# Optimization experiments

Hardware: AMD Instinct MI355X
Metric: run time of the kernel (lower is better)

## Reference

```python
import jax, jax.numpy as jnp
import numpy as np

EPS = 1e-5
OUTPUT_BINS = 1000


def _act_quant(x):
    # per-token absmax int8 quantization (BitNet b1.58)
    scale = 127.0 / jnp.clip(jnp.max(jnp.abs(x), axis=-1, keepdims=True), EPS, None)
    return jnp.clip(jnp.round(x * scale), -128.0, 127.0) / scale


def _weight_quant(w):
    # ternary absmean quantization
    scale = 1.0 / jnp.clip(jnp.mean(jnp.abs(w)), EPS, None)
    return jnp.clip(jnp.round(w * scale), -1.0, 1.0) / scale


def _ste(x, q):
    return x + jax.lax.stop_gradient(q - x)


def bitlinear(x, w):
    xq = _ste(x, _act_quant(x))
    wq = _ste(w, _weight_quant(w))
    return jnp.einsum('bi,oi->bo', xq, wq)


def layernorm(x, g, b):
    mu = jnp.mean(x, axis=-1, keepdims=True)
    var = jnp.mean(jnp.square(x - mu), axis=-1, keepdims=True)
    return (x - mu) * jax.lax.rsqrt(var + EPS) * g + b


def setup_inputs() -> dict:
    key = jax.random.key(0)
    ks = jax.random.split(key, 5)
    B, D_IN, H = 4096, 1024, 4096
    return {
        'x': jax.random.normal(ks[0], (B, D_IN), dtype=jnp.float32),
        'W0': jax.random.normal(ks[1], (H, D_IN), dtype=jnp.float32) * 0.02,
        'W1': jax.random.normal(ks[2], (H, H), dtype=jnp.float32) * 0.02,
        'W2': jax.random.normal(ks[3], (H, H), dtype=jnp.float32) * 0.02,
        'W3': jax.random.normal(ks[4], (2 * OUTPUT_BINS, H), dtype=jnp.float32) * 0.02,
        'g0': jnp.ones((H,), jnp.float32), 'b0': jnp.zeros((H,), jnp.float32),
        'g1': jnp.ones((H,), jnp.float32), 'b1': jnp.zeros((H,), jnp.float32),
        'g2': jnp.ones((H,), jnp.float32), 'b2': jnp.zeros((H,), jnp.float32),
    }


def reference(x, W0, W1, W2, W3, g0, b0, g1, b1, g2, b2):
    h = jax.nn.silu(layernorm(bitlinear(x, W0), g0, b0))
    h = jax.nn.silu(layernorm(bitlinear(h, W1), g1, b1))
    h = jax.nn.silu(layernorm(bitlinear(h, W2), g2, b2))
    out = bitlinear(h, W3)                      # [B, 2*output_bins]
    mz_logits, int_logits = jnp.split(out, 2, axis=-1)
    mz_values = jax.nn.sigmoid(mz_logits) * (OUTPUT_BINS - 1) + 1.0
    intensities = jax.nn.sigmoid(int_logits) * 100.0
    return (mz_values, intensities)
```

## Files before the change

### kernel.cpp

```cpp
#include <hip/hip_runtime.h>
#include <hip/hip_bf16.h>
#include <cstdint>
#include <cstddef>

#define EPS 1e-5f

typedef __attribute__((ext_vector_type(4))) int int32x4;

__device__ __forceinline__ float blk_sum(float v, float* s4) {
    #pragma unroll
    for (int o = 32; o; o >>= 1) v += __shfl_down(v, o, 64);
    if ((threadIdx.x & 63) == 0) s4[threadIdx.x >> 6] = v;
    __syncthreads();
    v = s4[0] + s4[1] + s4[2] + s4[3];
    __syncthreads();
    return v;
}

__device__ __forceinline__ void blk_sum2(float& a, float& b, float* s8) {
    #pragma unroll
    for (int o = 32; o; o >>= 1) {
        a += __shfl_down(a, o, 64);
        b += __shfl_down(b, o, 64);
    }
    if ((threadIdx.x & 63) == 0) {
        s8[threadIdx.x >> 6] = a;
        s8[4 + (threadIdx.x >> 6)] = b;
    }
    __syncthreads();
    a = s8[0] + s8[1] + s8[2] + s8[3];
    b = s8[4] + s8[5] + s8[6] + s8[7];
    __syncthreads();
}

__device__ __forceinline__ float blk_max(float v, float* s4) {
    #pragma unroll
    for (int o = 32; o; o >>= 1) v = fmaxf(v, __shfl_down(v, o, 64));
    if ((threadIdx.x & 63) == 0) s4[threadIdx.x >> 6] = v;
    __syncthreads();
    v = fmaxf(fmaxf(s4[0], s4[1]), fmaxf(s4[2], s4[3]));
    __syncthreads();
    return v;
}

__device__ __forceinline__ int pack4(float a, float b, float c, float d, float lo, float hi) {
    int x0 = (int)fminf(fmaxf(a, lo), hi);
    int x1 = (int)fminf(fmaxf(b, lo), hi);
    int x2 = (int)fminf(fmaxf(c, lo), hi);
    int x3 = (int)fminf(fmaxf(d, lo), hi);
    return (x0 & 255) | ((x1 & 255) << 8) | ((x2 & 255) << 16) | ((x3 & 255) << 24);
}

__device__ __forceinline__ float bflo(unsigned u) { return __uint_as_float(u << 16); }
__device__ __forceinline__ float bfhi(unsigned u) { return __uint_as_float(u & 0xffff0000u); }

__global__ __launch_bounds__(256) void absmean_all_kernel(
    const float* __restrict__ W0, const float* __restrict__ W1,
    const float* __restrict__ W2, const float* __restrict__ W3,
    float* __restrict__ part) {
    __shared__ float s4[4];
    const float* w; int sidx; unsigned rel;
    unsigned bx = blockIdx.x;
    if (bx < 1024)      { w = W0; sidx = 0; rel = bx; }
    else if (bx < 5120) { w = W1; sidx = 1; rel = bx - 1024; }
    else if (bx < 9216) { w = W2; sidx = 2; rel = bx - 5120; }
    else                { w = W3; sidx = 3; rel = bx - 9216; }
    const float4* p = (const float4*)w + (size_t)rel * 1024 + threadIdx.x;
    float4 v0 = p[0], v1 = p[256], v2 = p[512], v3 = p[768];
    float s = fabsf(v0.x) + fabsf(v0.y) + fabsf(v0.z) + fabsf(v0.w)
            + fabsf(v1.x) + fabsf(v1.y) + fabsf(v1.z) + fabsf(v1.w)
            + fabsf(v2.x) + fabsf(v2.y) + fabsf(v2.z) + fabsf(v2.w)
            + fabsf(v3.x) + fabsf(v3.y) + fabsf(v3.z) + fabsf(v3.w);
    s = blk_sum(s, s4);
    if (threadIdx.x == 0) atomicAdd(&part[(sidx * 64 + (rel & 63)) * 16], s);
}

__global__ __launch_bounds__(256) void reduce_sums_kernel(const float* __restrict__ part,
                                                          float* __restrict__ sums) {
    int w = threadIdx.x >> 6, l = threadIdx.x & 63;
    float v = part[(w * 64 + l) * 16];
    #pragma unroll
    for (int o = 32; o; o >>= 1) v += __shfl_down(v, o, 64);
    if (l == 0) sums[w] = v;
}

__global__ __launch_bounds__(256) void wquant_all_kernel(
    const float* __restrict__ W0, const float* __restrict__ W1,
    const float* __restrict__ W2, const float* __restrict__ W3,
    int* __restrict__ q0, int* __restrict__ q1, int* __restrict__ q2, int* __restrict__ q3,
    const float* __restrict__ sums) {
    const float* w; int* q; int sidx; unsigned rel; float invN; bool pad = false;
    unsigned bx = blockIdx.x;
    if (bx < 1024)      { w = W0; q = q0; sidx = 0; rel = bx;        invN = 1.f / 4194304.f; }
    else if (bx < 5120) { w = W1; q = q1; sidx = 1; rel = bx - 1024; invN = 1.f / 16777216.f; }
    else if (bx < 9216) { w = W2; q = q2; sidx = 2; rel = bx - 5120; invN = 1.f / 16777216.f; }
    else                { w = W3; q = q3; sidx = 3; rel = bx - 9216; invN = 1.f / 8192000.f;
                          pad = (rel >= 2000); }
    int4 o = {0, 0, 0, 0};
    if (!pad) {
        float mean = fmaxf(sums[sidx] * invN, EPS);
        float scale = 1.f / mean;
        const float4* p = (const float4*)w + (size_t)rel * 1024 + threadIdx.x * 4;
        float4 v0 = p[0], v1 = p[1], v2 = p[2], v3 = p[3];
        o.x = pack4(rintf(v0.x * scale), rintf(v0.y * scale), rintf(v0.z * scale), rintf(v0.w * scale), -1.f, 1.f);
        o.y = pack4(rintf(v1.x * scale), rintf(v1.y * scale), rintf(v1.z * scale), rintf(v1.w * scale), -1.f, 1.f);
        o.z = pack4(rintf(v2.x * scale), rintf(v2.y * scale), rintf(v2.z * scale), rintf(v2.w * scale), -1.f, 1.f);
        o.w = pack4(rintf(v3.x * scale), rintf(v3.y * scale), rintf(v3.z * scale), rintf(v3.w * scale), -1.f, 1.f);
    }
    ((int4*)q)[(size_t)rel * 256 + threadIdx.x] = o;
}

__global__ __launch_bounds__(256) void actquant_kernel(const float* __restrict__ x,
                                                       int* __restrict__ q,
                                                       float* __restrict__ inv_s) {
    __shared__ float s4[4];
    int row = blockIdx.x;
    const float4* xr = (const float4*)(x + (size_t)row * 1024);
    float4 v = xr[threadIdx.x];
    float m = fmaxf(fmaxf(fabsf(v.x), fabsf(v.y)), fmaxf(fabsf(v.z), fabsf(v.w)));
    m = blk_max(m, s4);
    m = fmaxf(m, EPS);
    float scale = 127.f / m;
    if (threadIdx.x == 0) inv_s[row] = m / 127.f;
    q[(size_t)row * 256 + threadIdx.x] =
        pack4(rintf(v.x * scale), rintf(v.y * scale),
              rintf(v.z * scale), rintf(v.w * scale), -128.f, 127.f);
}

__global__ __launch_bounds__(256) void ln_silu_quant_kernel(const ushort* __restrict__ h,
                                                            const float* __restrict__ g,
                                                            const float* __restrict__ b,
                                                            int* __restrict__ q,
                                                            float* __restrict__ inv_s) {
    __shared__ float s8[8];
    int row = blockIdx.x;
    int t = threadIdx.x;
    const uint4* hr = (const uint4*)(h + (size_t)row * 4096);
    uint4 p0 = hr[t * 2], p1 = hr[t * 2 + 1];
    float f[16];
    f[0] = bflo(p0.x); f[1] = bfhi(p0.x); f[2] = bflo(p0.y); f[3] = bfhi(p0.y);
    f[4] = bflo(p0.z); f[5] = bfhi(p0.z); f[6] = bflo(p0.w); f[7] = bfhi(p0.w);
    f[8] = bflo(p1.x); f[9] = bfhi(p1.x); f[10] = bflo(p1.y); f[11] = bfhi(p1.y);
    f[12] = bflo(p1.z); f[13] = bfhi(p1.z); f[14] = bflo(p1.w); f[15] = bfhi(p1.w);
    float sum = 0.f, sq = 0.f;
    #pragma unroll
    for (int i = 0; i < 16; i++) { sum += f[i]; sq += f[i] * f[i]; }
    blk_sum2(sum, sq, s8);
    float mu = sum * (1.f / 4096.f);
    float var = sq * (1.f / 4096.f) - mu * mu;
    float rs = rsqrtf(var + EPS);
    const float4* g4 = (const float4*)g;
    const float4* b4 = (const float4*)b;
    float amax = 0.f;
    #pragma unroll
    for (int i = 0; i < 4; i++) {
        float4 gg = g4[t * 4 + i];
        float4 bb = b4[t * 4 + i];
        float y0 = (f[i * 4 + 0] - mu) * rs * gg.x + bb.x;
        float y1 = (f[i * 4 + 1] - mu) * rs * gg.y + bb.y;
        float y2 = (f[i * 4 + 2] - mu) * rs * gg.z + bb.z;
        float y3 = (f[i * 4 + 3] - mu) * rs * gg.w + bb.w;
        f[i * 4 + 0] = y0 / (1.f + expf(-y0));
        f[i * 4 + 1] = y1 / (1.f + expf(-y1));
        f[i * 4 + 2] = y2 / (1.f + expf(-y2));
        f[i * 4 + 3] = y3 / (1.f + expf(-y3));
    }
    #pragma unroll
    for (int i = 0; i < 16; i++) amax = fmaxf(amax, fabsf(f[i]));
    amax = blk_max(amax, s8);
    amax = fmaxf(amax, EPS);
    float scale = 127.f / amax;
    if (t == 0) inv_s[row] = amax / 127.f;
    int4 o;
    o.x = pack4(rintf(f[0] * scale), rintf(f[1] * scale), rintf(f[2] * scale), rintf(f[3] * scale), -128.f, 127.f);
    o.y = pack4(rintf(f[4] * scale), rintf(f[5] * scale), rintf(f[6] * scale), rintf(f[7] * scale), -128.f, 127.f);
    o.z = pack4(rintf(f[8] * scale), rintf(f[9] * scale), rintf(f[10] * scale), rintf(f[11] * scale), -128.f, 127.f);
    o.w = pack4(rintf(f[12] * scale), rintf(f[13] * scale), rintf(f[14] * scale), rintf(f[15] * scale), -128.f, 127.f);
    ((int4*)((char*)q + (size_t)row * 4096))[t] = o;
}

__device__ __forceinline__ void load_lds16(const void* g, void* l) {
    __builtin_amdgcn_global_load_lds((__attribute__((address_space(1))) void*)(g),
                                     (__attribute__((address_space(3))) void*)(l), 16, 0, 0);
}

template <int MODE>
__global__ __launch_bounds__(256, 2) void gemm_i8_kernel(
    const char* __restrict__ A, const char* __restrict__ B,
    const float* __restrict__ inv_s, const float* __restrict__ wsum, float invWN,
    int K, void* __restrict__ outp) {
    __shared__ __align__(16) char lA[128 * 128];
    __shared__ __align__(16) char lB[128 * 128];
    const int t = threadIdx.x;
    const int lane = t & 63;
    const int wave = t >> 6;
    const int bm = blockIdx.y * 128, bn = blockIdx.x * 128;
    const int wr = (wave >> 1) * 64, wc = (wave & 1) * 64;

    int32x4 acc[4][4] = {};

    const int r0 = t >> 3;
    const int c0 = (t & 7) * 16;
    const int gcol = c0 ^ (16 * (r0 & 7));
    const char* gA = A + (size_t)(bm + r0) * K + gcol;
    const char* gB = B + (size_t)(bn + r0) * K + gcol;
    char* sA = lA + t * 16;
    char* sB = lB + t * 16;

    const int fr = lane & 15;
    const int fq = lane >> 4;
    const int swz = 16 * (fr & 7);

    for (int k0 = 0; k0 < K; k0 += 128) {
        #pragma unroll
        for (int j = 0; j < 4; j++)
            load_lds16(gA + (size_t)(j * 32) * K + k0, sA + j * 4096);
        #pragma unroll
        for (int j = 0; j < 4; j++)
            load_lds16(gB + (size_t)(j * 32) * K + k0, sB + j * 4096);
        __syncthreads();

        #pragma unroll
        for (int ks = 0; ks < 2; ks++) {
            const int col = (ks * 64 + fq * 16) ^ swz;
            int32x4 af[4], bf[4];
            #pragma unroll
            for (int mt = 0; mt < 4; mt++)
                af[mt] = *(const int32x4*)(lA + (wr + mt * 16 + fr) * 128 + col);
            #pragma unroll
            for (int nt = 0; nt < 4; nt++)
                bf[nt] = *(const int32x4*)(lB + (wc + nt * 16 + fr) * 128 + col);
            #pragma unroll
            for (int mt = 0; mt < 4; mt++) {
                #pragma unroll
                for (int nt = 0; nt < 4; nt++) {
                    acc[mt][nt] = __builtin_amdgcn_mfma_i32_16x16x64_i8(af[mt], bf[nt],
                                                                        acc[mt][nt], 0, 0, 0);
                }
            }
        }
        __syncthreads();
    }

    const float wmean = fmaxf(wsum[0] * invWN, EPS);
    #pragma unroll
    for (int mt = 0; mt < 4; mt++) {
        #pragma unroll
        for (int rg = 0; rg < 4; rg++) {
            int gr = bm + wr + mt * 16 + fq * 4 + rg;
            float rowscale = inv_s[gr] * wmean;
            #pragma unroll
            for (int nt = 0; nt < 4; nt++) {
                int gc = bn + wc + nt * 16 + fr;
                float v = (float)acc[mt][nt][rg] * rowscale;
                if (MODE == 0) {
                    ((__hip_bfloat16*)outp)[(size_t)gr * 4096 + gc] = __float2bfloat16(v);
                } else {
                    if (gc < 2000) {
                        float sg = 1.f / (1.f + expf(-v));
                        float* out = (float*)outp;
                        if (gc < 1000)
                            out[(size_t)gr * 1000 + gc] = sg * 999.f + 1.f;
                        else
                            out[(size_t)4096 * 1000 + (size_t)gr * 1000 + (gc - 1000)] =
                                sg * 100.f;
                    }
                }
            }
        }
    }
}

extern "C" void kernel_launch(void* const* d_in, const int* in_sizes, int n_in,
                              void* d_out, int out_size, void* d_ws, size_t ws_size,
                              hipStream_t stream) {
    const float* x  = (const float*)d_in[0];
    const float* W0 = (const float*)d_in[1];
    const float* W1 = (const float*)d_in[2];
    const float* W2 = (const float*)d_in[3];
    const float* W3 = (const float*)d_in[4];
    const float* g0 = (const float*)d_in[5];
    const float* b0 = (const float*)d_in[6];
    const float* g1 = (const float*)d_in[7];
    const float* b1 = (const float*)d_in[8];
    const float* g2 = (const float*)d_in[9];
    const float* b2 = (const float*)d_in[10];
    float* out = (float*)d_out;

    char* ws = (char*)d_ws;
    size_t off = 0;
    auto alloc = [&](size_t bytes) -> char* {
        char* p = ws + off;
        off = (off + bytes + 255) & ~(size_t)255;
        return p;
    };
    float* part = (float*)alloc(256 * 16 * sizeof(float));
    float* sums = (float*)alloc(4 * sizeof(float));
    float* inv0 = (float*)alloc(4096 * 4);
    float* inv1 = (float*)alloc(4096 * 4);
    float* inv2 = (float*)alloc(4096 * 4);
    float* inv3 = (float*)alloc(4096 * 4);
    char* wq0 = alloc(4096ll * 1024);
    char* wq1 = alloc(4096ll * 4096);
    char* wq2 = alloc(4096ll * 4096);
    char* wq3 = alloc(2048ll * 4096);
    char* a0  = alloc(4096ll * 1024);
    char* a1  = alloc(4096ll * 4096);
    char* a2  = alloc(4096ll * 4096);
    char* h   = alloc(4096ll * 4096 * 2);
    char* a3 = a1;

    hipMemsetAsync(part, 0, 256 * 16 * sizeof(float), stream);

    absmean_all_kernel<<<11216, 256, 0, stream>>>(W0, W1, W2, W3, part);
    reduce_sums_kernel<<<1, 256, 0, stream>>>(part, sums);
    actquant_kernel<<<4096, 256, 0, stream>>>(x, (int*)a0, inv0);
    wquant_all_kernel<<<11264, 256, 0, stream>>>(W0, W1, W2, W3, (int*)wq0, (int*)wq1,
                                                 (int*)wq2, (int*)wq3, sums);

    gemm_i8_kernel<0><<<dim3(32, 32), 256, 0, stream>>>(a0, wq0, inv0, sums + 0,
                                                        1.f / 4194304.f, 1024, h);
    ln_silu_quant_kernel<<<4096, 256, 0, stream>>>((const ushort*)h, g0, b0, (int*)a1, inv1);

    gemm_i8_kernel<0><<<dim3(32, 32), 256, 0, stream>>>(a1, wq1, inv1, sums + 1,
                                                        1.f / 16777216.f, 4096, h);
    ln_silu_quant_kernel<<<4096, 256, 0, stream>>>((const ushort*)h, g1, b1, (int*)a2, inv2);

    gemm_i8_kernel<0><<<dim3(32, 32), 256, 0, stream>>>(a2, wq2, inv2, sums + 2,
                                                        1.f / 16777216.f, 4096, h);
    ln_silu_quant_kernel<<<4096, 256, 0, stream>>>((const ushort*)h, g2, b2, (int*)a3, inv3);

    gemm_i8_kernel<1><<<dim3(16, 32), 256, 0, stream>>>(a3, wq3, inv3, sums + 3,
                                                        1.f / 8192000.f, 4096, out);
}
```

Baseline: 518.0 us.

## Add 256x256-tile 512-thread int8 MFMA GEMM with LDS double buffering for hidden layers

Adds a new int8 GEMM kernel that uses 256x256 output tiles per 8-wave workgroup, double-buffered LDS staging with direct global-to-LDS loads, XOR-swizzled LDS layout, interleaved MFMA/staging phases with s_setprio, and a workgroup index remap for L2 locality. The three 4096-wide hidden-layer GEMMs switch to it, while the final output GEMM stays on the old kernel. The aim is more operand reuse per LDS byte and better overlap of global loads with MFMA compute. The trade-offs are a grid of only 256 workgroups, which may not fill the device evenly, high register pressure from 32 accumulators per thread, and hand-written waitcnt counts that depend on how the compiler orders instructions.

```diff
diff --git a/kernel.cpp b/kernel.cpp
--- a/kernel.cpp
+++ b/kernel.cpp
@@ -271,6 +271,172 @@
     }
 }
 
+template <int MH>
+__device__ __forceinline__ void mfma_quad(int32x4 (&acc)[8][4], const int32x4 (&af)[4],
+                                          const int32x4 (&bf)[4]) {
+    #pragma unroll
+    for (int i = 0; i < 4; i++) {
+        #pragma unroll
+        for (int j = 0; j < 4; j++) {
+            acc[MH * 4 + i][j] =
+                __builtin_amdgcn_mfma_i32_16x16x64_i8(af[i], bf[j], acc[MH * 4 + i][j], 0, 0, 0);
+        }
+    }
+}
+
+__global__ __launch_bounds__(512, 2) void gemm_i8_big(
+    const char* __restrict__ A, const char* __restrict__ B,
+    const float* __restrict__ inv_s, const float* __restrict__ wsum, float invWN,
+    int K, __hip_bfloat16* __restrict__ outp) {
+    __shared__ __align__(16) char lA[2][2][256][64];
+    __shared__ __align__(16) char lB[2][2][256][64];
+    const int t = threadIdx.x;
+    const int lane = t & 63;
+    const int wave = t >> 6;
+
+    const int nwg = gridDim.x * gridDim.y;
+    const int wg0 = blockIdx.y * gridDim.x + blockIdx.x;
+    const int q8 = nwg >> 3;
+    const int wg = (wg0 & 7) * q8 + (wg0 >> 3);
+    const int bm = (wg / gridDim.x) * 256;
+    const int bn = (wg % gridDim.x) * 256;
+
+    const int wr = (wave >> 2) * 128;
+    const int wc = (wave & 3) * 64;
+
+    const int fr = lane & 15;
+    const int fq = lane >> 4;
+    const int rchunk = (fq ^ ((fr >> 1) & 3)) * 16;
+    const char* aRd = &lA[0][0][0][0] + (wr + fr) * 64 + rchunk;
+    const char* bRd = &lB[0][0][0][0] + (wc + fr) * 64 + rchunk;
+
+    const int srow = t >> 2;
+    const int schunk = ((t & 3) ^ ((t >> 3) & 3)) * 16;
+    const char* gA = A + (size_t)(bm + srow) * K + schunk;
+    const char* gB = B + (size_t)(bn + srow) * K + schunk;
+    char* sAd = &lA[0][0][0][0] + t * 16;
+    char* sBd = &lB[0][0][0][0] + t * 16;
+
+    int32x4 acc[8][4] = {};
+    int32x4 af[4], bf[4];
+
+    const int NT = K >> 7;
+
+#define STAGE_A(bb, kh, kt) \
+    load_lds16(gA + (size_t)(kt) * 128 + (kh) * 64, sAd + (bb) * 32768 + (kh) * 16384); \
+    load_lds16(gA + (size_t)128 * K + (size_t)(kt) * 128 + (kh) * 64, \
+               sAd + (bb) * 32768 + (kh) * 16384 + 8192);
+#define STAGE_B(bb, kh, kt) \
+    load_lds16(gB + (size_t)(kt) * 128 + (kh) * 64, sBd + (bb) * 32768 + (kh) * 16384); \
+    load_lds16(gB + (size_t)128 * K + (size_t)(kt) * 128 + (kh) * 64, \
+               sBd + (bb) * 32768 + (kh) * 16384 + 8192);
+#define LD_AF(bb, ks, mh) { \
+    const char* p_ = aRd + (bb) * 32768 + (ks) * 16384 + (mh) * 4096; \
+    af[0] = *(const int32x4*)(p_); \
+    af[1] = *(const int32x4*)(p_ + 1024); \
+    af[2] = *(const int32x4*)(p_ + 2048); \
+    af[3] = *(const int32x4*)(p_ + 3072); }
+#define LD_BF(bb, ks) { \
+    const char* p_ = bRd + (bb) * 32768 + (ks) * 16384; \
+    bf[0] = *(const int32x4*)(p_); \
+    bf[1] = *(const int32x4*)(p_ + 1024); \
+    bf[2] = *(const int32x4*)(p_ + 2048); \
+    bf[3] = *(const int32x4*)(p_ + 3072); }
+
+    STAGE_A(0, 0, 0); STAGE_B(0, 0, 0); STAGE_A(0, 1, 0); STAGE_B(0, 1, 0);
+    asm volatile("s_waitcnt vmcnt(4)" ::: "memory");
+    __builtin_amdgcn_s_barrier();
+
+    for (int kt = 0; kt < NT - 1; ++kt) {
+        const int b = kt & 1, nb = b ^ 1;
+        LD_BF(b, 0); LD_AF(b, 0, 0);
+        STAGE_A(nb, 0, kt + 1);
+        __builtin_amdgcn_s_barrier();
+        asm volatile("s_waitcnt lgkmcnt(0)" ::: "memory");
+        __builtin_amdgcn_s_setprio(1);
+        mfma_quad<0>(acc, af, bf);
+        __builtin_amdgcn_s_setprio(0);
+        __builtin_amdgcn_s_barrier();
+        LD_AF(b, 0, 1);
+        STAGE_B(nb, 0, kt + 1);
+        __builtin_amdgcn_s_barrier();
+        asm volatile("s_waitcnt lgkmcnt(0)" ::: "memory");
+        __builtin_amdgcn_s_setprio(1);
+        mfma_quad<1>(acc, af, bf);
+        __builtin_amdgcn_s_setprio(0);
+        asm volatile("s_waitcnt vmcnt(4)" ::: "memory");
+        __builtin_amdgcn_s_barrier();
+        LD_BF(b, 1); LD_AF(b, 1, 0);
+        STAGE_A(nb, 1, kt + 1);
+        __builtin_amdgcn_s_barrier();
+        asm volatile("s_waitcnt lgkmcnt(0)" ::: "memory");
+        __builtin_amdgcn_s_setprio(1);
+        mfma_quad<0>(acc, af, bf);
+        __builtin_amdgcn_s_setprio(0);
+        __builtin_amdgcn_s_barrier();
+        LD_AF(b, 1, 1);
+        STAGE_B(nb, 1, kt + 1);
+        __builtin_amdgcn_s_barrier();
+        asm volatile("s_waitcnt lgkmcnt(0)" ::: "memory");
+        __builtin_amdgcn_s_setprio(1);
+        mfma_quad<1>(acc, af, bf);
+        __builtin_amdgcn_s_setprio(0);
+        asm volatile("s_waitcnt vmcnt(4)" ::: "memory");
+        __builtin_amdgcn_s_barrier();
+    }
+
+    {
+        const int b = (NT - 1) & 1;
+        LD_BF(b, 0); LD_AF(b, 0, 0);
+        __builtin_amdgcn_s_barrier();
+        asm volatile("s_waitcnt lgkmcnt(0)" ::: "memory");
+        __builtin_amdgcn_s_setprio(1);
+        mfma_quad<0>(acc, af, bf);
+        __builtin_amdgcn_s_setprio(0);
+        __builtin_amdgcn_s_barrier();
+        LD_AF(b, 0, 1);
+        __builtin_amdgcn_s_barrier();
+        asm volatile("s_waitcnt lgkmcnt(0)" ::: "memory");
+        __builtin_amdgcn_s_setprio(1);
+        mfma_quad<1>(acc, af, bf);
+        __builtin_amdgcn_s_setprio(0);
+        asm volatile("s_waitcnt vmcnt(0)" ::: "memory");
+        __builtin_amdgcn_s_barrier();
+        LD_BF(b, 1); LD_AF(b, 1, 0);
+        __builtin_amdgcn_s_barrier();
+        asm volatile("s_waitcnt lgkmcnt(0)" ::: "memory");
+        __builtin_amdgcn_s_setprio(1);
+        mfma_quad<0>(acc, af, bf);
+        __builtin_amdgcn_s_setprio(0);
+        __builtin_amdgcn_s_barrier();
+        LD_AF(b, 1, 1);
+        asm volatile("s_waitcnt lgkmcnt(0)" ::: "memory");
+        __builtin_amdgcn_s_setprio(1);
+        mfma_quad<1>(acc, af, bf);
+        __builtin_amdgcn_s_setprio(0);
+    }
+#undef STAGE_A
+#undef STAGE_B
+#undef LD_AF
+#undef LD_BF
+
+    const float wmean = fmaxf(wsum[0] * invWN, EPS);
+    #pragma unroll
+    for (int mt = 0; mt < 8; mt++) {
+        #pragma unroll
+        for (int rg = 0; rg < 4; rg++) {
+            const int gr = bm + wr + mt * 16 + fq * 4 + rg;
+            const float rowscale = inv_s[gr] * wmean;
+            #pragma unroll
+            for (int nt = 0; nt < 4; nt++) {
+                const int gc = bn + wc + nt * 16 + fr;
+                outp[(size_t)gr * 4096 + gc] =
+                    __float2bfloat16((float)acc[mt][nt][rg] * rowscale);
+            }
+        }
+    }
+}
+
 extern "C" void kernel_launch(void* const* d_in, const int* in_sizes, int n_in,
                               void* d_out, int out_size, void* d_ws, size_t ws_size,
                               hipStream_t stream) {
@@ -318,16 +484,19 @@
     wquant_all_kernel<<<11264, 256, 0, stream>>>(W0, W1, W2, W3, (int*)wq0, (int*)wq1,
                                                  (int*)wq2, (int*)wq3, sums);
 
-    gemm_i8_kernel<0><<<dim3(32, 32), 256, 0, stream>>>(a0, wq0, inv0, sums + 0,
-                                                        1.f / 4194304.f, 1024, h);
+    gemm_i8_big<<<dim3(16, 16), 512, 0, stream>>>(a0, wq0, inv0, sums + 0,
+                                                  1.f / 4194304.f, 1024,
+                                                  (__hip_bfloat16*)h);
     ln_silu_quant_kernel<<<4096, 256, 0, stream>>>((const ushort*)h, g0, b0, (int*)a1, inv1);
 
-    gemm_i8_kernel<0><<<dim3(32, 32), 256, 0, stream>>>(a1, wq1, inv1, sums + 1,
-                                                        1.f / 16777216.f, 4096, h);
+    gemm_i8_big<<<dim3(16, 16), 512, 0, stream>>>(a1, wq1, inv1, sums + 1,
+                                                  1.f / 16777216.f, 4096,
+                                                  (__hip_bfloat16*)h);
     ln_silu_quant_kernel<<<4096, 256, 0, stream>>>((const ushort*)h, g1, b1, (int*)a2, inv2);
 
-    gemm_i8_kernel<0><<<dim3(32, 32), 256, 0, stream>>>(a2, wq2, inv2, sums + 2,
-                                                        1.f / 16777216.f, 4096, h);
+    gemm_i8_big<<<dim3(16, 16), 512, 0, stream>>>(a2, wq2, inv2, sums + 2,
+                                                  1.f / 16777216.f, 4096,
+                                                  (__hip_bfloat16*)h);
     ln_silu_quant_kernel<<<4096, 256, 0, stream>>>((const ushort*)h, g2, b2, (int*)a3, inv3);
 
     gemm_i8_kernel<1><<<dim3(16, 32), 256, 0, stream>>>(a3, wq3, inv3, sums + 3,
```

Measured after the change: 541.9 us. 4.6% more time.

## Add deep-pipelined 256x256 int8 MFMA GEMM for hidden layers

Applied to the files above, without the earlier changes.

Adds a new int8 GEMM kernel for the three hidden-layer matmuls. It uses 256x256 tiles with 512 threads and a 4-stage LDS ring filled by direct global-to-LDS loads. Register fragments are double-buffered, waitcnt and barrier scheduling is explicit, MFMA runs at raised priority, and workgroups are remapped across XCDs for cache locality. The goal is to hide memory latency behind MFMA and raise reuse per tile. The cost is 64KB of LDS and high register pressure, which limits occupancy, and the hand-tuned schedule is fragile. The loop assumes K is a multiple of 256 with at least 8 tiles, which holds for K=1024 and K=4096.

```diff
diff --git a/kernel.cpp b/kernel.cpp
--- a/kernel.cpp
+++ b/kernel.cpp
@@ -271,6 +271,136 @@
     }
 }
 
+template <int MH>
+__device__ __forceinline__ void mfma_quad(int32x4 (&acc)[8][4], const int32x4 (&af)[4],
+                                          const int32x4 (&bf)[4]) {
+    #pragma unroll
+    for (int i = 0; i < 4; i++) {
+        #pragma unroll
+        for (int j = 0; j < 4; j++) {
+            acc[MH * 4 + i][j] =
+                __builtin_amdgcn_mfma_i32_16x16x64_i8(af[i], bf[j], acc[MH * 4 + i][j], 0, 0, 0);
+        }
+    }
+}
+
+__global__ __launch_bounds__(512, 2) void gemm_i8_pipe(
+    const char* __restrict__ A, const char* __restrict__ B,
+    const float* __restrict__ inv_s, const float* __restrict__ wsum, float invWN,
+    int K, __hip_bfloat16* __restrict__ outp) {
+    __shared__ __align__(16) char lA[4][256][64];
+    __shared__ __align__(16) char lB[4][256][64];
+    const int t = threadIdx.x;
+    const int lane = t & 63;
+    const int wave = t >> 6;
+
+    const int nwg = gridDim.x * gridDim.y;
+    const int wg0 = blockIdx.y * gridDim.x + blockIdx.x;
+    const int q8 = nwg >> 3;
+    const int wg = (wg0 & 7) * q8 + (wg0 >> 3);
+    const int bm = (wg / gridDim.x) * 256;
+    const int bn = (wg % gridDim.x) * 256;
+
+    const int wr = (wave >> 2) * 128;
+    const int wc = (wave & 3) * 64;
+    const int fr = lane & 15;
+    const int fq = lane >> 4;
+
+    const int srow = t >> 2;
+    const char* gA = A + (size_t)(bm + srow) * K + (t & 3) * 16;
+    const char* gB = B + (size_t)(bn + srow) * K + (t & 3) * 16;
+    char* sAd = &lA[0][0][0] + t * 16;
+    char* sBd = &lB[0][0][0] + t * 16;
+
+    const char* aRd = &lA[0][0][0] + (wr + fr) * 64 + fq * 16;
+    const char* bRd = &lB[0][0][0] + (wc + fr) * 64 + fq * 16;
+
+    int32x4 acc[8][4] = {};
+    int32x4 afX[4], afY[4], bfX[4], bfY[4];
+    const int NT = K >> 6;
+
+#define STAGE_A(buf, kt) { \
+    load_lds16(gA + (size_t)(kt) * 64, sAd + (buf) * 16384); \
+    load_lds16(gA + (size_t)128 * K + (size_t)(kt) * 64, sAd + (buf) * 16384 + 8192); }
+#define STAGE_B(buf, kt) { \
+    load_lds16(gB + (size_t)(kt) * 64, sBd + (buf) * 16384); \
+    load_lds16(gB + (size_t)128 * K + (size_t)(kt) * 64, sBd + (buf) * 16384 + 8192); }
+#define LD_AF(dst, buf, mh) { \
+    const char* p_ = aRd + (buf) * 16384 + (mh) * 4096; \
+    dst[0] = *(const int32x4*)(p_); \
+    dst[1] = *(const int32x4*)(p_ + 1024); \
+    dst[2] = *(const int32x4*)(p_ + 2048); \
+    dst[3] = *(const int32x4*)(p_ + 3072); }
+#define LD_BF(dst, buf) { \
+    const char* p_ = bRd + (buf) * 16384; \
+    dst[0] = *(const int32x4*)(p_); \
+    dst[1] = *(const int32x4*)(p_ + 1024); \
+    dst[2] = *(const int32x4*)(p_ + 2048); \
+    dst[3] = *(const int32x4*)(p_ + 3072); }
+#define WAITL(n) { asm volatile("s_waitcnt lgkmcnt(" #n ")" ::: "memory"); \
+                   __builtin_amdgcn_sched_barrier(0); }
+#define WAITV(n) { asm volatile("s_waitcnt vmcnt(" #n ")" ::: "memory"); \
+                   __builtin_amdgcn_sched_barrier(0); }
+#define BAR() { __builtin_amdgcn_s_barrier(); __builtin_amdgcn_sched_barrier(0); }
+#define MF0(afc, bfc) { __builtin_amdgcn_s_setprio(1); mfma_quad<0>(acc, afc, bfc); \
+                        __builtin_amdgcn_s_setprio(0); }
+#define MF1(afc, bfc) { __builtin_amdgcn_s_setprio(1); mfma_quad<1>(acc, afc, bfc); \
+                        __builtin_amdgcn_s_setprio(0); }
+
+    STAGE_A(0, 0); STAGE_B(0, 0);
+    STAGE_A(1, 1); STAGE_B(1, 1);
+    STAGE_A(2, 2); STAGE_B(2, 2);
+    WAITV(8);
+    BAR();
+    LD_BF(bfX, 0); LD_AF(afX, 0, 0);
+
+    for (int kt = 0; kt <= NT - 8; kt += 4) {
+        STAGE_A(3, kt + 3); LD_AF(afY, 0, 1); WAITL(4); MF0(afX, bfX); WAITV(6); BAR();
+        STAGE_B(3, kt + 3); LD_BF(bfY, 1); LD_AF(afX, 1, 0); WAITL(8); MF1(afY, bfX); BAR();
+        STAGE_A(0, kt + 4); LD_AF(afY, 1, 1); WAITL(4); MF0(afX, bfY); WAITV(6); BAR();
+        STAGE_B(0, kt + 4); LD_BF(bfX, 2); LD_AF(afX, 2, 0); WAITL(8); MF1(afY, bfY); BAR();
+        STAGE_A(1, kt + 5); LD_AF(afY, 2, 1); WAITL(4); MF0(afX, bfX); WAITV(6); BAR();
+        STAGE_B(1, kt + 5); LD_BF(bfY, 3); LD_AF(afX, 3, 0); WAITL(8); MF1(afY, bfX); BAR();
+        STAGE_A(2, kt + 6); LD_AF(afY, 3, 1); WAITL(4); MF0(afX, bfY); WAITV(6); BAR();
+        STAGE_B(2, kt + 6); LD_BF(bfX, 0); LD_AF(afX, 0, 0); WAITL(8); MF1(afY, bfY); BAR();
+    }
+
+    STAGE_A(3, NT - 1); LD_AF(afY, 0, 1); WAITL(4); MF0(afX, bfX); WAITV(6); BAR();
+    STAGE_B(3, NT - 1); LD_BF(bfY, 1); LD_AF(afX, 1, 0); WAITL(8); MF1(afY, bfX); BAR();
+    LD_AF(afY, 1, 1); WAITL(4); MF0(afX, bfY); WAITV(4); BAR();
+    LD_BF(bfX, 2); LD_AF(afX, 2, 0); WAITL(8); MF1(afY, bfY); BAR();
+    LD_AF(afY, 2, 1); WAITL(4); MF0(afX, bfX); WAITV(0); BAR();
+    LD_BF(bfY, 3); LD_AF(afX, 3, 0); WAITL(8); MF1(afY, bfX); BAR();
+    LD_AF(afY, 3, 1); WAITL(4); MF0(afX, bfY); BAR();
+    WAITL(0); MF1(afY, bfY);
+
+#undef STAGE_A
+#undef STAGE_B
+#undef LD_AF
+#undef LD_BF
+#undef WAITL
+#undef WAITV
+#undef BAR
+#undef MF0
+#undef MF1
+
+    const float wmean = fmaxf(wsum[0] * invWN, EPS);
+    #pragma unroll
+    for (int mt = 0; mt < 8; mt++) {
+        #pragma unroll
+        for (int rg = 0; rg < 4; rg++) {
+            const int gr = bm + wr + mt * 16 + fq * 4 + rg;
+            const float rowscale = inv_s[gr] * wmean;
+            #pragma unroll
+            for (int nt = 0; nt < 4; nt++) {
+                const int gc = bn + wc + nt * 16 + fr;
+                outp[(size_t)gr * 4096 + gc] =
+                    __float2bfloat16((float)acc[mt][nt][rg] * rowscale);
+            }
+        }
+    }
+}
+
 extern "C" void kernel_launch(void* const* d_in, const int* in_sizes, int n_in,
                               void* d_out, int out_size, void* d_ws, size_t ws_size,
                               hipStream_t stream) {
@@ -318,16 +448,19 @@
     wquant_all_kernel<<<11264, 256, 0, stream>>>(W0, W1, W2, W3, (int*)wq0, (int*)wq1,
                                                  (int*)wq2, (int*)wq3, sums);
 
-    gemm_i8_kernel<0><<<dim3(32, 32), 256, 0, stream>>>(a0, wq0, inv0, sums + 0,
-                                                        1.f / 4194304.f, 1024, h);
+    gemm_i8_pipe<<<dim3(16, 16), 512, 0, stream>>>(a0, wq0, inv0, sums + 0,
+                                                   1.f / 4194304.f, 1024,
+                                                   (__hip_bfloat16*)h);
     ln_silu_quant_kernel<<<4096, 256, 0, stream>>>((const ushort*)h, g0, b0, (int*)a1, inv1);
 
-    gemm_i8_kernel<0><<<dim3(32, 32), 256, 0, stream>>>(a1, wq1, inv1, sums + 1,
-                                                        1.f / 16777216.f, 4096, h);
+    gemm_i8_pipe<<<dim3(16, 16), 512, 0, stream>>>(a1, wq1, inv1, sums + 1,
+                                                   1.f / 16777216.f, 4096,
+                                                   (__hip_bfloat16*)h);
     ln_silu_quant_kernel<<<4096, 256, 0, stream>>>((const ushort*)h, g1, b1, (int*)a2, inv2);
 
-    gemm_i8_kernel<0><<<dim3(32, 32), 256, 0, stream>>>(a2, wq2, inv2, sums + 2,
-                                                        1.f / 16777216.f, 4096, h);
+    gemm_i8_pipe<<<dim3(16, 16), 512, 0, stream>>>(a2, wq2, inv2, sums + 2,
+                                                   1.f / 16777216.f, 4096,
+                                                   (__hip_bfloat16*)h);
     ln_silu_quant_kernel<<<4096, 256, 0, stream>>>((const ushort*)h, g2, b2, (int*)a3, inv3);
 
     gemm_i8_kernel<1><<<dim3(16, 32), 256, 0, stream>>>(a3, wq3, inv3, sums + 3,
```

New measurement: 522.9 us. Within noise of the previous version (+0.9%).

## Pipeline int8 GEMM with 4-stage LDS buffering, register double-buffering, and XCD remap

Applied to the files above, without the earlier changes.

Replaces the single-buffered int8 MFMA GEMM with a 4-stage software pipeline over 64-wide K tiles. Global-to-LDS loads are issued three tiles ahead, LDS fragments are double-buffered in registers, and explicit waitcnt, barriers and setprio are used to overlap memory with MFMA. It also remaps workgroup IDs across the 8 XCDs and uses a new LDS swizzle for the 64-byte rows. The aim is to hide load latency and avoid the two full barriers per K step, at the cost of hand-tuned wait counts that are fragile and a loop that assumes NT is a multiple of 4 and at least 8.

```diff
diff --git a/kernel.cpp b/kernel.cpp
--- a/kernel.cpp
+++ b/kernel.cpp
@@ -184,74 +184,132 @@
                                      (__attribute__((address_space(3))) void*)(l), 16, 0, 0);
 }
 
+__device__ __forceinline__ void mfma_16(int32x4 (&acc)[4][4], const int32x4 (&af)[4],
+                                        const int32x4 (&bf)[4]) {
+    #pragma unroll
+    for (int i = 0; i < 4; i++) {
+        #pragma unroll
+        for (int j = 0; j < 4; j++) {
+            acc[i][j] =
+                __builtin_amdgcn_mfma_i32_16x16x64_i8(af[i], bf[j], acc[i][j], 0, 0, 0);
+        }
+    }
+}
+
 template <int MODE>
-__global__ __launch_bounds__(256, 2) void gemm_i8_kernel(
+__global__ __launch_bounds__(256, 2) void gemm_i8_pipe(
     const char* __restrict__ A, const char* __restrict__ B,
     const float* __restrict__ inv_s, const float* __restrict__ wsum, float invWN,
     int K, void* __restrict__ outp) {
-    __shared__ __align__(16) char lA[128 * 128];
-    __shared__ __align__(16) char lB[128 * 128];
+    __shared__ __align__(16) char lA[4][128][64];
+    __shared__ __align__(16) char lB[4][128][64];
     const int t = threadIdx.x;
     const int lane = t & 63;
     const int wave = t >> 6;
-    const int bm = blockIdx.y * 128, bn = blockIdx.x * 128;
-    const int wr = (wave >> 1) * 64, wc = (wave & 1) * 64;
-
-    int32x4 acc[4][4] = {};
-
-    const int r0 = t >> 3;
-    const int c0 = (t & 7) * 16;
-    const int gcol = c0 ^ (16 * (r0 & 7));
-    const char* gA = A + (size_t)(bm + r0) * K + gcol;
-    const char* gB = B + (size_t)(bn + r0) * K + gcol;
-    char* sA = lA + t * 16;
-    char* sB = lB + t * 16;
-
+
+    const int nwg = gridDim.x * gridDim.y;
+    const int wg0 = blockIdx.y * gridDim.x + blockIdx.x;
+    const int q8 = nwg >> 3;
+    const int wg = (wg0 & 7) * q8 + (wg0 >> 3);
+    const int bm = (wg / gridDim.x) * 128;
+    const int bn = (wg % gridDim.x) * 128;
+
+    const int wr = (wave >> 1) * 64;
+    const int wc = (wave & 1) * 64;
     const int fr = lane & 15;
     const int fq = lane >> 4;
-    const int swz = 16 * (fr & 7);
-
-    for (int k0 = 0; k0 < K; k0 += 128) {
-        #pragma unroll
-        for (int j = 0; j < 4; j++)
-            load_lds16(gA + (size_t)(j * 32) * K + k0, sA + j * 4096);
-        #pragma unroll
-        for (int j = 0; j < 4; j++)
-            load_lds16(gB + (size_t)(j * 32) * K + k0, sB + j * 4096);
-        __syncthreads();
-
-        #pragma unroll
-        for (int ks = 0; ks < 2; ks++) {
-            const int col = (ks * 64 + fq * 16) ^ swz;
-            int32x4 af[4], bf[4];
-            #pragma unroll
-            for (int mt = 0; mt < 4; mt++)
-                af[mt] = *(const int32x4*)(lA + (wr + mt * 16 + fr) * 128 + col);
-            #pragma unroll
-            for (int nt = 0; nt < 4; nt++)
-                bf[nt] = *(const int32x4*)(lB + (wc + nt * 16 + fr) * 128 + col);
-            #pragma unroll
-            for (int mt = 0; mt < 4; mt++) {
-                #pragma unroll
-                for (int nt = 0; nt < 4; nt++) {
-                    acc[mt][nt] = __builtin_amdgcn_mfma_i32_16x16x64_i8(af[mt], bf[nt],
-                                                                        acc[mt][nt], 0, 0, 0);
-                }
-            }
-        }
-        __syncthreads();
-    }
+
+    const int srow = t >> 2;
+    const int schunk = ((t & 3) ^ ((t >> 3) & 3)) * 16;
+    const char* gA = A + (size_t)(bm + srow) * K + schunk;
+    const char* gB = B + (size_t)(bn + srow) * K + schunk;
+    char* sAd = &lA[0][0][0] + t * 16;
+    char* sBd = &lB[0][0][0] + t * 16;
+
+    const int rchunk = (fq ^ ((fr >> 1) & 3)) * 16;
+    const char* aRd = &lA[0][0][0] + (wr + fr) * 64 + rchunk;
+    const char* bRd = &lB[0][0][0] + (wc + fr) * 64 + rchunk;
+
+    int32x4 acc[4][4] = {};
+    int32x4 afX[4], afY[4], bfX[4], bfY[4];
+    const int NT = K >> 6;
+
+#define STAGE_A(buf, kt) { \
+    load_lds16(gA + (size_t)(kt) * 64, sAd + (buf) * 8192); \
+    load_lds16(gA + (size_t)64 * K + (size_t)(kt) * 64, sAd + (buf) * 8192 + 4096); }
+#define STAGE_B(buf, kt) { \
+    load_lds16(gB + (size_t)(kt) * 64, sBd + (buf) * 8192); \
+    load_lds16(gB + (size_t)64 * K + (size_t)(kt) * 64, sBd + (buf) * 8192 + 4096); }
+#define LD_AF(dst, buf) { \
+    const char* p_ = aRd + (buf) * 8192; \
+    dst[0] = *(const int32x4*)(p_); \
+    dst[1] = *(const int32x4*)(p_ + 1024); \
+    dst[2] = *(const int32x4*)(p_ + 2048); \
+    dst[3] = *(const int32x4*)(p_ + 3072); }
+#define LD_BF(dst, buf) { \
+    const char* p_ = bRd + (buf) * 8192; \
+    dst[0] = *(const int32x4*)(p_); \
+    dst[1] = *(const int32x4*)(p_ + 1024); \
+    dst[2] = *(const int32x4*)(p_ + 2048); \
+    dst[3] = *(const int32x4*)(p_ + 3072); }
+#define WAITL(n) { asm volatile("s_waitcnt lgkmcnt(" #n ")" ::: "memory"); \
+                   __builtin_amdgcn_sched_barrier(0); }
+#define WAITV(n) { asm volatile("s_waitcnt vmcnt(" #n ")" ::: "memory"); \
+                   __builtin_amdgcn_sched_barrier(0); }
+#define BAR() { __builtin_amdgcn_s_barrier(); __builtin_amdgcn_sched_barrier(0); }
+#define MF(afc, bfc) { __builtin_amdgcn_s_setprio(1); mfma_16(acc, afc, bfc); \
+                       __builtin_amdgcn_s_setprio(0); }
+
+    STAGE_A(0, 0); STAGE_B(0, 0);
+    STAGE_A(1, 1); STAGE_B(1, 1);
+    STAGE_A(2, 2); STAGE_B(2, 2);
+    WAITV(4);
+    BAR();
+    LD_AF(afX, 0); LD_BF(bfX, 0);
+
+    for (int kt = 0; kt <= NT - 8; kt += 4) {
+        STAGE_A(3, kt + 3); STAGE_B(3, kt + 3);
+        LD_AF(afY, 1); LD_BF(bfY, 1);
+        WAITL(8); MF(afX, bfX); WAITV(4); BAR();
+        STAGE_A(0, kt + 4); STAGE_B(0, kt + 4);
+        LD_AF(afX, 2); LD_BF(bfX, 2);
+        WAITL(8); MF(afY, bfY); WAITV(4); BAR();
+        STAGE_A(1, kt + 5); STAGE_B(1, kt + 5);
+        LD_AF(afY, 3); LD_BF(bfY, 3);
+        WAITL(8); MF(afX, bfX); WAITV(4); BAR();
+        STAGE_A(2, kt + 6); STAGE_B(2, kt + 6);
+        LD_AF(afX, 0); LD_BF(bfX, 0);
+        WAITL(8); MF(afY, bfY); WAITV(4); BAR();
+    }
+
+    STAGE_A(3, NT - 1); STAGE_B(3, NT - 1);
+    LD_AF(afY, 1); LD_BF(bfY, 1);
+    WAITL(8); MF(afX, bfX); WAITV(4); BAR();
+    LD_AF(afX, 2); LD_BF(bfX, 2);
+    WAITL(8); MF(afY, bfY); WAITV(0); BAR();
+    LD_AF(afY, 3); LD_BF(bfY, 3);
+    WAITL(8); MF(afX, bfX);
+    WAITL(0); MF(afY, bfY);
+
+#undef STAGE_A
+#undef STAGE_B
+#undef LD_AF
+#undef LD_BF
+#undef WAITL
+#undef WAITV
+#undef BAR
+#undef MF
 
     const float wmean = fmaxf(wsum[0] * invWN, EPS);
     #pragma unroll
     for (int mt = 0; mt < 4; mt++) {
         #pragma unroll
         for (int rg = 0; rg < 4; rg++) {
-            int gr = bm + wr + mt * 16 + fq * 4 + rg;
-            float rowscale = inv_s[gr] * wmean;
+            const int gr = bm + wr + mt * 16 + fq * 4 + rg;
+            const float rowscale = inv_s[gr] * wmean;
             #pragma unroll
             for (int nt = 0; nt < 4; nt++) {
-                int gc = bn + wc + nt * 16 + fr;
+                const int gc = bn + wc + nt * 16 + fr;
                 float v = (float)acc[mt][nt][rg] * rowscale;
                 if (MODE == 0) {
                     ((__hip_bfloat16*)outp)[(size_t)gr * 4096 + gc] = __float2bfloat16(v);
@@ -318,18 +376,18 @@
     wquant_all_kernel<<<11264, 256, 0, stream>>>(W0, W1, W2, W3, (int*)wq0, (int*)wq1,
                                                  (int*)wq2, (int*)wq3, sums);
 
-    gemm_i8_kernel<0><<<dim3(32, 32), 256, 0, stream>>>(a0, wq0, inv0, sums + 0,
-                                                        1.f / 4194304.f, 1024, h);
+    gemm_i8_pipe<0><<<dim3(32, 32), 256, 0, stream>>>(a0, wq0, inv0, sums + 0,
+                                                      1.f / 4194304.f, 1024, h);
     ln_silu_quant_kernel<<<4096, 256, 0, stream>>>((const ushort*)h, g0, b0, (int*)a1, inv1);
 
-    gemm_i8_kernel<0><<<dim3(32, 32), 256, 0, stream>>>(a1, wq1, inv1, sums + 1,
-                                                        1.f / 16777216.f, 4096, h);
+    gemm_i8_pipe<0><<<dim3(32, 32), 256, 0, stream>>>(a1, wq1, inv1, sums + 1,
+                                                      1.f / 16777216.f, 4096, h);
     ln_silu_quant_kernel<<<4096, 256, 0, stream>>>((const ushort*)h, g1, b1, (int*)a2, inv2);
 
-    gemm_i8_kernel<0><<<dim3(32, 32), 256, 0, stream>>>(a2, wq2, inv2, sums + 2,
-                                                        1.f / 16777216.f, 4096, h);
+    gemm_i8_pipe<0><<<dim3(32, 32), 256, 0, stream>>>(a2, wq2, inv2, sums + 2,
+                                                      1.f / 16777216.f, 4096, h);
     ln_silu_quant_kernel<<<4096, 256, 0, stream>>>((const ushort*)h, g2, b2, (int*)a3, inv3);
 
-    gemm_i8_kernel<1><<<dim3(16, 32), 256, 0, stream>>>(a3, wq3, inv3, sums + 3,
-                                                        1.f / 8192000.f, 4096, out);
-}
+    gemm_i8_pipe<1><<<dim3(16, 32), 256, 0, stream>>>(a3, wq3, inv3, sums + 3,
+                                                      1.f / 8192000.f, 4096, out);
+}
```

Measured after the change: 551.5 us. +6.5%, slower.
